# Kernel tuning notes

Hardware: AMD Instinct MI355X
Metric: run time of the kernel (lower is better)

The kernel has to match this reference:

```python
import jax, jax.numpy as jnp
import numpy as np

N_NODES = 100000
N_EDGES = 1600000
IN_F = 256
OUT_F = 128


def setup_inputs() -> dict:
    key = jax.random.key(0)
    k1, k2, k3, k4, k5, k6 = jax.random.split(key, 6)
    init_range = float(np.sqrt(6.0 / (IN_F + OUT_F)))
    stdv = 1.0 / float(np.sqrt(OUT_F))
    return {
        "x": jax.random.normal(k1, (N_NODES, IN_F), dtype=jnp.float32),
        "weight": jax.random.uniform(k2, (IN_F, OUT_F), dtype=jnp.float32, minval=-init_range, maxval=init_range),
        "bias": jax.random.uniform(k3, (OUT_F,), dtype=jnp.float32, minval=-stdv, maxval=stdv),
        "adj_val": jax.random.uniform(k4, (N_EDGES,), dtype=jnp.float32),
        "adj_row": jax.random.randint(k5, (N_EDGES,), 0, N_NODES),  # destination node per edge
        "adj_col": jax.random.randint(k6, (N_EDGES,), 0, N_NODES),  # source node per edge
    }


def reference(x, weight, bias, adj_val, adj_row, adj_col):
    # support = X @ W   (dense GEMM, [N, in] x [in, out])
    support = x @ weight
    # output = spmm(adj, support): gather source rows, scale by edge value,
    # segment-sum into destination rows. Honors COO sparsity; no [N,N] dense.
    gathered = support[adj_col] * adj_val[:, None]          # [E, out]
    out = jax.ops.segment_sum(gathered, adj_row, num_segments=N_NODES)
    return out + bias
```

## Files before the change

kernel.cpp:

```cpp
#include <hip/hip_runtime.h>

#define N_NODES 100000
#define N_EDGES 1600000
#define IN_F 256
#define OUT_F 128

#define NBUCK 1563
#define FBUCK 64
#define CAP 1664

#define SORT_CHUNKS 128
#define CHUNK_E (N_EDGES / SORT_CHUNKS)

#define GEMM_BM 128
#define GEMM_BLOCKS ((N_NODES + GEMM_BM - 1) / GEMM_BM)

typedef __attribute__((ext_vector_type(8))) short bf16x8;
typedef __attribute__((ext_vector_type(4))) float f32x4;

__device__ __forceinline__ unsigned short f2bf(float f) {
    unsigned u = __float_as_uint(f);
    unsigned r = u + 0x7fffu + ((u >> 16) & 1u);
    return (unsigned short)(r >> 16);
}

__global__ __launch_bounds__(256) void wz_kernel(const float* __restrict__ w,
                                                 unsigned short* __restrict__ wt,
                                                 int* __restrict__ cursor) {
    const int tid = threadIdx.x;
    if (blockIdx.x < 128) {
        int c = blockIdx.x;
        wt[c * IN_F + tid] = f2bf(w[tid * OUT_F + c]);
    } else {
        int i = (blockIdx.x - 128) * 256 + tid;
        if (i < NBUCK) cursor[i] = 0;
    }
}

__global__ __launch_bounds__(512, 4) void gemm_sort_kernel(const float* __restrict__ x,
                                                           const unsigned short* __restrict__ wt,
                                                           unsigned short* __restrict__ support,
                                                           const int* __restrict__ rowi,
                                                           const int* __restrict__ coli,
                                                           const float* __restrict__ val,
                                                           int* __restrict__ cursor,
                                                           uint2* __restrict__ tmp) {
    __shared__ unsigned short ws[128 * 256];
    __shared__ int bh[NBUCK];

    const int tid = threadIdx.x;

    if (blockIdx.x < SORT_CHUNKS) {
        const int c = blockIdx.x;
        for (int i = tid; i < NBUCK; i += 512) bh[i] = 0;
        __syncthreads();
        const int e0 = c * CHUNK_E;
        for (int i = tid; i < CHUNK_E; i += 512)
            atomicAdd(&bh[rowi[e0 + i] >> 6], 1);
        __syncthreads();
        for (int i = tid; i < NBUCK; i += 512) {
            int n = bh[i];
            bh[i] = n ? atomicAdd(&cursor[i], n) : 0;
        }
        __syncthreads();
        for (int i = tid; i < CHUNK_E; i += 512) {
            int e = e0 + i;
            int dst = rowi[e];
            int b = dst >> 6;
            int pos = atomicAdd(&bh[b], 1);
            tmp[(size_t)b * CAP + pos] =
                make_uint2(((unsigned)(dst & 63) << 17) | (unsigned)coli[e],
                           __float_as_uint(val[e]));
        }
        return;
    }

    const int lane = tid & 63;
    const int wv = tid >> 6;
    const int row0 = (blockIdx.x - SORT_CHUNKS) * GEMM_BM;
    const int l15 = lane & 15;
    const int kq = lane >> 4;

    int arow = row0 + wv * 16 + l15;
    if (arow > N_NODES - 1) arow = N_NODES - 1;
    const float* xrow = &x[(size_t)arow * IN_F + kq * 8];

    f32x4 a[16];
#pragma unroll
    for (int kt = 0; kt < 8; ++kt) {
        asm volatile("global_load_dwordx4 %0, %1, off"
                     : "=v"(a[2 * kt + 0]) : "v"(xrow + kt * 32));
        asm volatile("global_load_dwordx4 %0, %1, off"
                     : "=v"(a[2 * kt + 1]) : "v"(xrow + kt * 32 + 4));
    }

#pragma unroll
    for (int it = 0; it < 8; ++it) {
        int ci = it * 512 + tid;
        int col = ci >> 5, ch = ci & 31;
        uint4 v = *reinterpret_cast<const uint4*>(&wt[col * IN_F + ch * 8]);
        int slot = ch ^ (col & 7);
        *reinterpret_cast<uint4*>(&ws[col * 256 + slot * 8]) = v;
    }

    asm volatile("s_waitcnt vmcnt(0)" ::: "memory");
    __builtin_amdgcn_sched_barrier(0);
    __syncthreads();

    f32x4 acc[8];
#pragma unroll
    for (int n = 0; n < 8; ++n) acc[n] = (f32x4){0.f, 0.f, 0.f, 0.f};

#pragma unroll
    for (int kt = 0; kt < 8; ++kt) {
        f32x4 a0 = a[2 * kt + 0];
        f32x4 a1 = a[2 * kt + 1];
        bf16x8 af;
        af[0] = (short)f2bf(a0[0]); af[1] = (short)f2bf(a0[1]);
        af[2] = (short)f2bf(a0[2]); af[3] = (short)f2bf(a0[3]);
        af[4] = (short)f2bf(a1[0]); af[5] = (short)f2bf(a1[1]);
        af[6] = (short)f2bf(a1[2]); af[7] = (short)f2bf(a1[3]);
#pragma unroll
        for (int n = 0; n < 8; ++n) {
            int col = n * 16 + l15;
            int slot = (kt * 4 + kq) ^ (col & 7);
            bf16x8 bfv = *reinterpret_cast<const bf16x8*>(&ws[col * 256 + slot * 8]);
            acc[n] = __builtin_amdgcn_mfma_f32_16x16x32_bf16(af, bfv, acc[n], 0, 0, 0);
        }
    }

#pragma unroll
    for (int r = 0; r < 4; ++r) {
        int row = row0 + wv * 16 + kq * 4 + r;
        if (row < N_NODES) {
#pragma unroll
            for (int n = 0; n < 8; ++n) {
                support[(size_t)row * OUT_F + n * 16 + l15] = f2bf(acc[n][r]);
            }
        }
    }
}

__global__ __launch_bounds__(256) void fine_accum_kernel(const unsigned short* __restrict__ support,
                                                         const uint2* __restrict__ tmp,
                                                         const int* __restrict__ cursor,
                                                         const float* __restrict__ bias,
                                                         float* __restrict__ out) {
    __shared__ uint2 plds[CAP];
    __shared__ int hist[FBUCK];
    __shared__ int scanb[FBUCK];
    __shared__ int cur[FBUCK];

    const int tid = threadIdx.x, b = blockIdx.x;
    const int cnt = cursor[b];
    const size_t base = (size_t)b * CAP;

    if (tid < FBUCK) hist[tid] = 0;
    __syncthreads();
    for (int i = tid; i < cnt; i += 256) {
        unsigned long long uu = __builtin_nontemporal_load(
            reinterpret_cast<const unsigned long long*>(&tmp[base + i]));
        atomicAdd(&hist[(unsigned)(uu & 0xffffffffu) >> 17], 1);
    }
    __syncthreads();
    if (tid < FBUCK) scanb[tid] = hist[tid];
    __syncthreads();
#pragma unroll
    for (int off = 1; off < FBUCK; off <<= 1) {
        int t = (tid < FBUCK && tid >= off) ? scanb[tid - off] : 0;
        __syncthreads();
        if (tid < FBUCK) scanb[tid] += t;
        __syncthreads();
    }
    if (tid < FBUCK) cur[tid] = scanb[tid] - hist[tid];
    __syncthreads();
    for (int i = tid; i < cnt; i += 256) {
        unsigned long long uu = __builtin_nontemporal_load(
            reinterpret_cast<const unsigned long long*>(&tmp[base + i]));
        unsigned ux = (unsigned)(uu & 0xffffffffu);
        int dl = ux >> 17;
        int pos = atomicAdd(&cur[dl], 1);
        plds[pos] = make_uint2(ux & 0x1FFFFu, (unsigned)(uu >> 32));
    }
    __syncthreads();

    const int lane = tid & 63;
    const int wv = tid >> 6;
    const int grp = lane >> 4;
    const int l16 = lane & 15;

    float4 b0 = *reinterpret_cast<const float4*>(&bias[l16 * 8]);
    float4 b1 = *reinterpret_cast<const float4*>(&bias[l16 * 8 + 4]);

    for (int ni = 0; ni < 16; ++ni) {
        const int dl = wv * 16 + ni;
        const int node = b * FBUCK + dl;
        if (node >= N_NODES) break;
        const int s = (dl == 0) ? 0 : scanb[dl - 1];
        const int e = scanb[dl];

        float acc[8];
#pragma unroll
        for (int t = 0; t < 8; ++t) acc[t] = 0.f;

        int j = s + grp;
        for (; j + 4 < e; j += 8) {
            uint2 p0 = plds[j];
            uint2 p1 = plds[j + 4];
            uint4 s0 = *reinterpret_cast<const uint4*>(&support[(size_t)p0.x * OUT_F + l16 * 8]);
            uint4 s1 = *reinterpret_cast<const uint4*>(&support[(size_t)p1.x * OUT_F + l16 * 8]);
            float v0 = __uint_as_float(p0.y);
            float v1 = __uint_as_float(p1.y);
            unsigned u0[4] = {s0.x, s0.y, s0.z, s0.w};
            unsigned u1[4] = {s1.x, s1.y, s1.z, s1.w};
#pragma unroll
            for (int q = 0; q < 4; ++q) {
                acc[2 * q + 0] += __uint_as_float(u0[q] << 16) * v0;
                acc[2 * q + 1] += __uint_as_float(u0[q] & 0xffff0000u) * v0;
                acc[2 * q + 0] += __uint_as_float(u1[q] << 16) * v1;
                acc[2 * q + 1] += __uint_as_float(u1[q] & 0xffff0000u) * v1;
            }
        }
        for (; j < e; j += 4) {
            uint2 p0 = plds[j];
            uint4 s0 = *reinterpret_cast<const uint4*>(&support[(size_t)p0.x * OUT_F + l16 * 8]);
            float v0 = __uint_as_float(p0.y);
            unsigned u0[4] = {s0.x, s0.y, s0.z, s0.w};
#pragma unroll
            for (int q = 0; q < 4; ++q) {
                acc[2 * q + 0] += __uint_as_float(u0[q] << 16) * v0;
                acc[2 * q + 1] += __uint_as_float(u0[q] & 0xffff0000u) * v0;
            }
        }

#pragma unroll
        for (int t = 0; t < 8; ++t) {
            acc[t] += __shfl_xor(acc[t], 16);
            acc[t] += __shfl_xor(acc[t], 32);
        }

        if (grp == 0) {
            f32x4 o0 = {acc[0] + b0.x, acc[1] + b0.y, acc[2] + b0.z, acc[3] + b0.w};
            f32x4 o1 = {acc[4] + b1.x, acc[5] + b1.y, acc[6] + b1.z, acc[7] + b1.w};
            f32x4* op = reinterpret_cast<f32x4*>(&out[(size_t)node * OUT_F + l16 * 8]);
            __builtin_nontemporal_store(o0, op);
            __builtin_nontemporal_store(o1, op + 1);
        }
    }
}

extern "C" void kernel_launch(void* const* d_in, const int* in_sizes, int n_in,
                              void* d_out, int out_size, void* d_ws, size_t ws_size,
                              hipStream_t stream) {
    const float* x       = (const float*)d_in[0];
    const float* weight  = (const float*)d_in[1];
    const float* bias    = (const float*)d_in[2];
    const float* adj_val = (const float*)d_in[3];
    const int*   adj_row = (const int*)d_in[4];
    const int*   adj_col = (const int*)d_in[5];
    float* out = (float*)d_out;

    unsigned short* support = (unsigned short*)d_ws;
    unsigned short* wt = support + (size_t)N_NODES * OUT_F;
    int* cursor = (int*)(wt + IN_F * OUT_F);
    uint2* tmp = (uint2*)(cursor + 1564);

    wz_kernel<<<128 + 7, 256, 0, stream>>>(weight, wt, cursor);
    gemm_sort_kernel<<<SORT_CHUNKS + GEMM_BLOCKS, 512, 0, stream>>>(
        x, wt, support, adj_row, adj_col, adj_val, cursor, tmp);
    fine_accum_kernel<<<NBUCK, 256, 0, stream>>>(support, tmp, cursor, bias, out);
}
```

Baseline: 118.7 us.

## Split fused gemm/sort kernel into separate sort and GEMM kernels

Breaks the combined kernel, where some blocks bucket-sorted edges and the rest ran the bf16 MFMA GEMM, into two kernels launched one after the other. The sort now uses 256 chunks with 256 threads per block, and the GEMM no longer reserves shared memory for the sort histogram. The GEMM also drops the inline-asm prefetch of X rows ahead of the W staging and loads X inside the k-loop. This gives up the overlap of sort and GEMM and adds a launch, in exchange for lighter per-block resource use in each kernel.

```diff
diff --git a/kernel.cpp b/kernel.cpp
--- a/kernel.cpp
+++ b/kernel.cpp
@@ -9,7 +9,7 @@
 #define FBUCK 64
 #define CAP 1664
 
-#define SORT_CHUNKS 128
+#define SORT_CHUNKS 256
 #define CHUNK_E (N_EDGES / SORT_CHUNKS)
 
 #define GEMM_BM 128
@@ -37,62 +37,46 @@
     }
 }
 
-__global__ __launch_bounds__(512, 4) void gemm_sort_kernel(const float* __restrict__ x,
-                                                           const unsigned short* __restrict__ wt,
-                                                           unsigned short* __restrict__ support,
-                                                           const int* __restrict__ rowi,
-                                                           const int* __restrict__ coli,
-                                                           const float* __restrict__ val,
-                                                           int* __restrict__ cursor,
-                                                           uint2* __restrict__ tmp) {
+__global__ __launch_bounds__(256) void sort_kernel(const int* __restrict__ rowi,
+                                                   const int* __restrict__ coli,
+                                                   const float* __restrict__ val,
+                                                   int* __restrict__ cursor,
+                                                   uint2* __restrict__ tmp) {
+    __shared__ int bh[NBUCK];
+    const int tid = threadIdx.x, c = blockIdx.x;
+    for (int i = tid; i < NBUCK; i += 256) bh[i] = 0;
+    __syncthreads();
+    const int e0 = c * CHUNK_E;
+    for (int i = tid; i < CHUNK_E; i += 256)
+        atomicAdd(&bh[rowi[e0 + i] >> 6], 1);
+    __syncthreads();
+    for (int i = tid; i < NBUCK; i += 256) {
+        int n = bh[i];
+        bh[i] = n ? atomicAdd(&cursor[i], n) : 0;
+    }
+    __syncthreads();
+    for (int i = tid; i < CHUNK_E; i += 256) {
+        int e = e0 + i;
+        int dst = rowi[e];
+        int b = dst >> 6;
+        int pos = atomicAdd(&bh[b], 1);
+        tmp[(size_t)b * CAP + pos] =
+            make_uint2(((unsigned)(dst & 63) << 17) | (unsigned)coli[e],
+                       __float_as_uint(val[e]));
+    }
+}
+
+__global__ __launch_bounds__(512, 4) void gemm_kernel(const float* __restrict__ x,
+                                                      const unsigned short* __restrict__ wt,
+                                                      unsigned short* __restrict__ support) {
     __shared__ unsigned short ws[128 * 256];
-    __shared__ int bh[NBUCK];
 
     const int tid = threadIdx.x;
-
-    if (blockIdx.x < SORT_CHUNKS) {
-        const int c = blockIdx.x;
-        for (int i = tid; i < NBUCK; i += 512) bh[i] = 0;
-        __syncthreads();
-        const int e0 = c * CHUNK_E;
-        for (int i = tid; i < CHUNK_E; i += 512)
-            atomicAdd(&bh[rowi[e0 + i] >> 6], 1);
-        __syncthreads();
-        for (int i = tid; i < NBUCK; i += 512) {
-            int n = bh[i];
-            bh[i] = n ? atomicAdd(&cursor[i], n) : 0;
-        }
-        __syncthreads();
-        for (int i = tid; i < CHUNK_E; i += 512) {
-            int e = e0 + i;
-            int dst = rowi[e];
-            int b = dst >> 6;
-            int pos = atomicAdd(&bh[b], 1);
-            tmp[(size_t)b * CAP + pos] =
-                make_uint2(((unsigned)(dst & 63) << 17) | (unsigned)coli[e],
-                           __float_as_uint(val[e]));
-        }
-        return;
-    }
-
     const int lane = tid & 63;
     const int wv = tid >> 6;
-    const int row0 = (blockIdx.x - SORT_CHUNKS) * GEMM_BM;
+    const int row0 = blockIdx.x * GEMM_BM;
     const int l15 = lane & 15;
     const int kq = lane >> 4;
-
-    int arow = row0 + wv * 16 + l15;
-    if (arow > N_NODES - 1) arow = N_NODES - 1;
-    const float* xrow = &x[(size_t)arow * IN_F + kq * 8];
-
-    f32x4 a[16];
-#pragma unroll
-    for (int kt = 0; kt < 8; ++kt) {
-        asm volatile("global_load_dwordx4 %0, %1, off"
-                     : "=v"(a[2 * kt + 0]) : "v"(xrow + kt * 32));
-        asm volatile("global_load_dwordx4 %0, %1, off"
-                     : "=v"(a[2 * kt + 1]) : "v"(xrow + kt * 32 + 4));
-    }
 
 #pragma unroll
     for (int it = 0; it < 8; ++it) {
@@ -102,10 +86,11 @@
         int slot = ch ^ (col & 7);
         *reinterpret_cast<uint4*>(&ws[col * 256 + slot * 8]) = v;
     }
-
-    asm volatile("s_waitcnt vmcnt(0)" ::: "memory");
-    __builtin_amdgcn_sched_barrier(0);
-    __syncthreads();
+    __syncthreads();
+
+    int arow = row0 + wv * 16 + l15;
+    if (arow > N_NODES - 1) arow = N_NODES - 1;
+    const float* xrow = &x[(size_t)arow * IN_F + kq * 8];
 
     f32x4 acc[8];
 #pragma unroll
@@ -113,8 +98,8 @@
 
 #pragma unroll
     for (int kt = 0; kt < 8; ++kt) {
-        f32x4 a0 = a[2 * kt + 0];
-        f32x4 a1 = a[2 * kt + 1];
+        f32x4 a0 = *reinterpret_cast<const f32x4*>(xrow + kt * 32);
+        f32x4 a1 = *reinterpret_cast<const f32x4*>(xrow + kt * 32 + 4);
         bf16x8 af;
         af[0] = (short)f2bf(a0[0]); af[1] = (short)f2bf(a0[1]);
         af[2] = (short)f2bf(a0[2]); af[3] = (short)f2bf(a0[3]);
@@ -266,7 +251,7 @@
     uint2* tmp = (uint2*)(cursor + 1564);
 
     wz_kernel<<<128 + 7, 256, 0, stream>>>(weight, wt, cursor);
-    gemm_sort_kernel<<<SORT_CHUNKS + GEMM_BLOCKS, 512, 0, stream>>>(
-        x, wt, support, adj_row, adj_col, adj_val, cursor, tmp);
+    sort_kernel<<<SORT_CHUNKS, 256, 0, stream>>>(adj_row, adj_col, adj_val, cursor, tmp);
+    gemm_kernel<<<GEMM_BLOCKS, 512, 0, stream>>>(x, wt, support);
     fine_accum_kernel<<<NBUCK, 256, 0, stream>>>(support, tmp, cursor, bias, out);
 }
```

After: 136.3 us. 14.8% more time.
